# Kernel tuning notes

Hardware: AMD Instinct MI355X
Metric: run time of the kernel (lower is better)

The kernel has to match this reference:

```python
import jax, jax.numpy as jnp
import numpy as np

NUM_SCOPES, NUM_DECOMPS, BATCH, NODES_IN, NUM_SUMS = 128, 8, 1024, 32, 32


def logmatmul(a, b):
    """Stable log-domain matmul: out[..., b, j] = logsumexp_k(a[..., b, k] + b[..., k, j]).
    a: [s, d, B, K], b: [s, d, K, J] -> [s, d, B, J]."""
    max_a = jnp.max(a, axis=-1, keepdims=True)            # [s, d, B, 1]
    max_b = jnp.max(b, axis=-2, keepdims=True)            # [s, d, 1, J]
    prod = jnp.einsum('sdbk,sdkj->sdbj', jnp.exp(a - max_a), jnp.exp(b - max_b))
    return jnp.log(prod) + max_a + max_b


def setup_inputs() -> dict:
    key = jax.random.key(0)
    k1, k2 = jax.random.split(key)
    x = jax.random.normal(k1, (NUM_SCOPES, NUM_DECOMPS, BATCH, NODES_IN), dtype=jnp.float32)
    # accumulators are linear-space (logspace_accumulators=False) and must be > 0
    accumulators = jax.random.uniform(
        k2, (NUM_SCOPES, NUM_DECOMPS, NODES_IN, NUM_SUMS),
        minval=0.1, maxval=1.0, dtype=jnp.float32)
    return {"x": x, "accumulators": accumulators}


def reference(x, accumulators):
    # log_softmax over the nodes_in axis (axis=2) of log(accumulators)
    log_weights = jax.nn.log_softmax(jnp.log(accumulators), axis=2)
    return logmatmul(x, log_weights)  # [s, d, B, num_sums]
```

## Files before the change

### kernel.cpp

```cpp
#include <hip/hip_runtime.h>


#define KDIM 32
#define JDIM 32
#define ROWS 256
#define THREADS 256
#define XPAD 33

__global__ __launch_bounds__(THREADS, 4) void sws_kernel(
    const float* __restrict__ x,
    const float* __restrict__ acc,
    float* __restrict__ out)
{
    __shared__ float w_lds[KDIM * JDIM];
    __shared__ float inv_lds[JDIM];
    __shared__ float x_lds[ROWS * XPAD];

    const int t   = threadIdx.x;
    const int blk = blockIdx.x;
    const int sd  = blk >> 2;

    const float4* x4     = (const float4*)(x + (size_t)blk * ROWS * KDIM);
    const float*  a_base = acc + (size_t)sd * (KDIM * JDIM);

    float4 xv4[8];
#pragma unroll
    for (int i = 0; i < 8; ++i) xv4[i] = x4[t + i * THREADS];

    {
        float av[4];
#pragma unroll
        for (int i = 0; i < 4; ++i) av[i] = a_base[t + i * THREADS];
#pragma unroll
        for (int i = 0; i < 4; ++i) w_lds[t + i * THREADS] = av[i];
    }
    __syncthreads();
    if (t < JDIM) {
        float s = 0.f;
#pragma unroll
        for (int k = 0; k < KDIM; ++k) s += w_lds[k * JDIM + t];
        inv_lds[t] = 1.0f / s;
    }
    __syncthreads();
#pragma unroll
    for (int i = 0; i < 4; ++i) {
        int idx = t + i * THREADS;
        w_lds[idx] *= inv_lds[idx & (JDIM - 1)];
    }

#pragma unroll
    for (int i = 0; i < 8; ++i) {
        int f   = t + i * THREADS;
        int row = f >> 3;
        int c   = (f & 7) * 4;
        float* p = &x_lds[row * XPAD + c];
        p[0] = xv4[i].x; p[1] = xv4[i].y; p[2] = xv4[i].z; p[3] = xv4[i].w;
    }
    __syncthreads();

    float e[KDIM];
#pragma unroll
    for (int k = 0; k < KDIM; ++k) e[k] = x_lds[t * XPAD + k];

    float m = e[0];
#pragma unroll
    for (int k = 1; k < KDIM; ++k) m = fmaxf(m, e[k]);
#pragma unroll
    for (int k = 0; k < KDIM; ++k) e[k] = __expf(e[k] - m);

    float accv[JDIM];
#pragma unroll
    for (int j = 0; j < JDIM; ++j) accv[j] = 0.f;

#pragma unroll
    for (int k = 0; k < KDIM; ++k) {
        float ek = e[k];
        const float4* wr = (const float4*)(w_lds + k * JDIM);
#pragma unroll
        for (int j4 = 0; j4 < 8; ++j4) {
            float4 w = wr[j4];
            accv[4 * j4 + 0] = fmaf(ek, w.x, accv[4 * j4 + 0]);
            accv[4 * j4 + 1] = fmaf(ek, w.y, accv[4 * j4 + 1]);
            accv[4 * j4 + 2] = fmaf(ek, w.z, accv[4 * j4 + 2]);
            accv[4 * j4 + 3] = fmaf(ek, w.w, accv[4 * j4 + 3]);
        }
    }

    float4* o4 = (float4*)(out + (size_t)blk * ROWS * KDIM + (size_t)t * KDIM);
#pragma unroll
    for (int j4 = 0; j4 < 8; ++j4) {
        float4 o;
        o.x = __logf(accv[4 * j4 + 0]) + m;
        o.y = __logf(accv[4 * j4 + 1]) + m;
        o.z = __logf(accv[4 * j4 + 2]) + m;
        o.w = __logf(accv[4 * j4 + 3]) + m;
        o4[j4] = o;
    }
}

extern "C" void kernel_launch(void* const* d_in, const int* in_sizes, int n_in,
                              void* d_out, int out_size, void* d_ws, size_t ws_size,
                              hipStream_t stream) {
    const float* x   = (const float*)d_in[0];
    const float* acc = (const float*)d_in[1];
    float* out = (float*)d_out;

    dim3 grid(4096);
    dim3 block(THREADS);
    hipLaunchKernelGGL(sws_kernel, grid, block, 0, stream, x, acc, out);
}
```

Baseline: 245.7 us.

## Compute log-matmul with bf16 MFMA instead of scalar FP32 FMAs

```diff
diff --git a/kernel.cpp b/kernel.cpp
--- a/kernel.cpp
+++ b/kernel.cpp
@@ -1,100 +1,121 @@
 #include <hip/hip_runtime.h>
+#include <stdint.h>
 
 
-#define KDIM 32
-#define JDIM 32
-#define ROWS 256
 #define THREADS 256
-#define XPAD 33
+#define ROWS    256
+#define EPITCH  40
+#define WPITCH  40
+
+typedef __attribute__((ext_vector_type(8))) short short8;
+typedef __attribute__((ext_vector_type(4))) float f32x4;
+
+__device__ __forceinline__ uint32_t pack2_bf16(float lo, float hi) {
+    uint32_t ul = __builtin_bit_cast(uint32_t, lo);
+    uint32_t uh = __builtin_bit_cast(uint32_t, hi);
+    ul = (ul + 0x7fffu + ((ul >> 16) & 1u)) >> 16;
+    uh = (uh + 0x7fffu + ((uh >> 16) & 1u)) >> 16;
+    return ul | (uh << 16);
+}
 
 __global__ __launch_bounds__(THREADS, 4) void sws_kernel(
     const float* __restrict__ x,
     const float* __restrict__ acc,
     float* __restrict__ out)
 {
-    __shared__ float w_lds[KDIM * JDIM];
-    __shared__ float inv_lds[JDIM];
-    __shared__ float x_lds[ROWS * XPAD];
+    __shared__ float w_f32[32 * 32];
+    __shared__ float inv_lds[32];
+    __shared__ float m_lds[ROWS];
+    __shared__ __align__(16) unsigned short e_lds[ROWS * EPITCH];
+    __shared__ __align__(16) unsigned short wt_lds[32 * WPITCH];
 
-    const int t   = threadIdx.x;
-    const int blk = blockIdx.x;
-    const int sd  = blk >> 2;
+    const int t    = threadIdx.x;
+    const int blk  = blockIdx.x;
+    const int sd   = blk >> 2;
+    const int lane = t & 63;
+    const int wv   = t >> 6;
+    const int l15  = lane & 15;
+    const int quad = lane >> 4;
 
-    const float4* x4     = (const float4*)(x + (size_t)blk * ROWS * KDIM);
-    const float*  a_base = acc + (size_t)sd * (KDIM * JDIM);
+    const float4* x4 = (const float4*)(x + (size_t)blk * ROWS * 32);
+    float4 xv[8];
+#pragma unroll
+    for (int i = 0; i < 8; ++i) xv[i] = x4[t + i * THREADS];
 
-    float4 xv4[8];
-#pragma unroll
-    for (int i = 0; i < 8; ++i) xv4[i] = x4[t + i * THREADS];
-
+    const float* a_base = acc + (size_t)sd * (32 * 32);
     {
         float av[4];
 #pragma unroll
         for (int i = 0; i < 4; ++i) av[i] = a_base[t + i * THREADS];
 #pragma unroll
-        for (int i = 0; i < 4; ++i) w_lds[t + i * THREADS] = av[i];
+        for (int i = 0; i < 4; ++i) w_f32[t + i * THREADS] = av[i];
     }
     __syncthreads();
-    if (t < JDIM) {
+    if (t < 32) {
         float s = 0.f;
 #pragma unroll
-        for (int k = 0; k < KDIM; ++k) s += w_lds[k * JDIM + t];
+        for (int k = 0; k < 32; ++k) s += w_f32[k * 32 + t];
         inv_lds[t] = 1.0f / s;
     }
     __syncthreads();
 #pragma unroll
     for (int i = 0; i < 4; ++i) {
         int idx = t + i * THREADS;
-        w_lds[idx] *= inv_lds[idx & (JDIM - 1)];
+        int k = idx >> 5, j = idx & 31;
+        float v = w_f32[idx] * inv_lds[j];
+        uint32_t u = __builtin_bit_cast(uint32_t, v);
+        u = (u + 0x7fffu + ((u >> 16) & 1u)) >> 16;
+        wt_lds[j * WPITCH + k] = (unsigned short)u;
     }
 
 #pragma unroll
     for (int i = 0; i < 8; ++i) {
-        int f   = t + i * THREADS;
-        int row = f >> 3;
-        int c   = (f & 7) * 4;
-        float* p = &x_lds[row * XPAD + c];
-        p[0] = xv4[i].x; p[1] = xv4[i].y; p[2] = xv4[i].z; p[3] = xv4[i].w;
+        float4 v = xv[i];
+        float m = fmaxf(fmaxf(v.x, v.y), fmaxf(v.z, v.w));
+        m = fmaxf(m, __shfl_xor(m, 1, 64));
+        m = fmaxf(m, __shfl_xor(m, 2, 64));
+        m = fmaxf(m, __shfl_xor(m, 4, 64));
+        int f = t + i * THREADS;
+        int row = f >> 3, c4 = f & 7;
+        uint32_t p0 = pack2_bf16(__expf(v.x - m), __expf(v.y - m));
+        uint32_t p1 = pack2_bf16(__expf(v.z - m), __expf(v.w - m));
+        *(uint2*)&e_lds[row * EPITCH + c4 * 4] = make_uint2(p0, p1);
+        if (c4 == 0) m_lds[row] = m;
     }
     __syncthreads();
 
-    float e[KDIM];
+    short8 bfrag[2];
 #pragma unroll
-    for (int k = 0; k < KDIM; ++k) e[k] = x_lds[t * XPAD + k];
+    for (int jt = 0; jt < 2; ++jt)
+        bfrag[jt] = *(const short8*)&wt_lds[(jt * 16 + l15) * WPITCH + quad * 8];
 
-    float m = e[0];
+    f32x4 cacc[4][2];
 #pragma unroll
-    for (int k = 1; k < KDIM; ++k) m = fmaxf(m, e[k]);
+    for (int rt4 = 0; rt4 < 4; ++rt4) {
+        int rt = wv * 4 + rt4;
+        short8 afrag = *(const short8*)&e_lds[(rt * 16 + l15) * EPITCH + quad * 8];
 #pragma unroll
-    for (int k = 0; k < KDIM; ++k) e[k] = __expf(e[k] - m);
-
-    float accv[JDIM];
-#pragma unroll
-    for (int j = 0; j < JDIM; ++j) accv[j] = 0.f;
-
-#pragma unroll
-    for (int k = 0; k < KDIM; ++k) {
-        float ek = e[k];
-        const float4* wr = (const float4*)(w_lds + k * JDIM);
-#pragma unroll
-        for (int j4 = 0; j4 < 8; ++j4) {
-            float4 w = wr[j4];
-            accv[4 * j4 + 0] = fmaf(ek, w.x, accv[4 * j4 + 0]);
-            accv[4 * j4 + 1] = fmaf(ek, w.y, accv[4 * j4 + 1]);
-            accv[4 * j4 + 2] = fmaf(ek, w.z, accv[4 * j4 + 2]);
-            accv[4 * j4 + 3] = fmaf(ek, w.w, accv[4 * j4 + 3]);
-        }
+        for (int jt = 0; jt < 2; ++jt)
+            cacc[rt4][jt] = __builtin_amdgcn_mfma_f32_16x16x32_bf16(
+                afrag, bfrag[jt], (f32x4){0.f, 0.f, 0.f, 0.f}, 0, 0, 0);
     }
 
-    float4* o4 = (float4*)(out + (size_t)blk * ROWS * KDIM + (size_t)t * KDIM);
+    float* obase = out + (size_t)blk * ROWS * 32;
 #pragma unroll
-    for (int j4 = 0; j4 < 8; ++j4) {
-        float4 o;
-        o.x = __logf(accv[4 * j4 + 0]) + m;
-        o.y = __logf(accv[4 * j4 + 1]) + m;
-        o.z = __logf(accv[4 * j4 + 2]) + m;
-        o.w = __logf(accv[4 * j4 + 3]) + m;
-        o4[j4] = o;
+    for (int rt4 = 0; rt4 < 4; ++rt4) {
+        int rt = wv * 4 + rt4;
+        int r0 = rt * 16 + quad * 4;
+        float4 mv = *(const float4*)&m_lds[r0];
+        float mr[4] = {mv.x, mv.y, mv.z, mv.w};
+#pragma unroll
+        for (int jt = 0; jt < 2; ++jt) {
+            int col = jt * 16 + l15;
+#pragma unroll
+            for (int r = 0; r < 4; ++r) {
+                float val = __logf(cacc[rt4][jt][r]) + mr[r];
+                obase[(size_t)(r0 + r) * 32 + col] = val;
+            }
+        }
     }
 }
 
```

Result: faster. 235.6 us (-4.1%).
